# Kernel tuning notes

Measured on AMD Instinct MI355X. Metric: run time of the kernel, lower is better.

## Reference

```python
import jax, jax.numpy as jnp
from jax import lax
import numpy as np

KK = 9          # 3x3 kernel points
BN_EPS = 1e-5


def setup_inputs() -> dict:
    key = jax.random.key(0)
    ks = jax.random.split(key, 8)
    B, C, O, H, W = 4, 256, 256, 64, 64
    x = jax.random.normal(ks[0], (B, C, H, W), jnp.float32)
    # offset/mask conv: 27 = 2*9 offsets + 9 mask logits; small init so offsets are O(1) px
    w_off = jax.random.normal(ks[1], (3 * KK, C, 3, 3), jnp.float32) * 0.01
    b_off = jnp.zeros((3 * KK,), jnp.float32)
    # main deformable conv weight [O, C, 3, 3]
    w = jax.random.normal(ks[2], (O, C, 3, 3), jnp.float32) * (1.0 / np.sqrt(C * KK))
    b = jax.random.normal(ks[3], (O,), jnp.float32) * 0.01
    # BatchNorm (eval mode) params
    gamma = jax.random.uniform(ks[4], (O,), jnp.float32, 0.5, 1.5)
    beta = jax.random.normal(ks[5], (O,), jnp.float32) * 0.1
    running_mean = jax.random.normal(ks[6], (O,), jnp.float32) * 0.1
    running_var = jax.random.uniform(ks[7], (O,), jnp.float32, 0.5, 1.5)
    return dict(x=x, w_off=w_off, b_off=b_off, w=w, b=b, gamma=gamma,
                beta=beta, running_mean=running_mean, running_var=running_var)


def _bilinear_sample(x, py, px):
    """x: [B,C,H,W]; py/px: [B,KK,H,W] float sample coords -> [B,C,KK,H,W]."""
    B, C, H, W = x.shape
    xflat = x.reshape(B, C, H * W)
    y0 = jnp.floor(py)
    x0 = jnp.floor(px)
    ly = py - y0      # frac weights
    lx = px - x0
    y0i = y0.astype(jnp.int32)
    x0i = x0.astype(jnp.int32)

    def corner(yi, xi, wgt):
        valid = (yi >= 0) & (yi < H) & (xi >= 0) & (xi < W)  # zero padding outside
        idx = jnp.clip(yi, 0, H - 1) * W + jnp.clip(xi, 0, W - 1)
        v = jnp.take_along_axis(xflat, idx.reshape(B, 1, -1), axis=2)  # [B,C,KK*H*W]
        return v * (wgt * valid).reshape(B, 1, -1)

    out = (corner(y0i,     x0i,     (1 - ly) * (1 - lx))
           + corner(y0i,     x0i + 1, (1 - ly) * lx)
           + corner(y0i + 1, x0i,     ly * (1 - lx))
           + corner(y0i + 1, x0i + 1, ly * lx))
    return out.reshape(B, C, KK, H, W)


def _deform_conv_bn_relu(x, w_off, b_off, w, b, gamma, beta, running_mean, running_var):
    B, C, H, W = x.shape
    O = w.shape[0]
    # offset/mask branch: plain 3x3 conv, stride 1, pad 1
    om = lax.conv_general_dilated(x, w_off, (1, 1), [(1, 1), (1, 1)])
    om = om + b_off[None, :, None, None]              # [B, 27, H, W]
    off_y = om[:, :KK]                                # DCNv2: o1 -> y offsets
    off_x = om[:, KK:2 * KK]                          # o2 -> x offsets
    mask = jax.nn.sigmoid(om[:, 2 * KK:])             # [B, 9, H, W]

    # base sampling grid for each of the 9 kernel taps (stride 1, pad 1)
    k = jnp.arange(KK)
    ki = (k // 3)[None, :, None, None].astype(jnp.float32)
    kj = (k % 3)[None, :, None, None].astype(jnp.float32)
    hh = jnp.arange(H, dtype=jnp.float32)[None, None, :, None]
    ww = jnp.arange(W, dtype=jnp.float32)[None, None, None, :]
    py = hh - 1.0 + ki + off_y                        # [B,9,H,W]
    px = ww - 1.0 + kj + off_x

    sampled = _bilinear_sample(x, py, px)             # [B,C,9,H,W]
    sampled = sampled * mask[:, None]                 # modulated (DCNv2)

    out = jnp.einsum('bckhw,ock->bohw', sampled, w.reshape(O, C, KK))
    out = out + b[None, :, None, None]

    # BatchNorm (eval / running stats) + ReLU
    inv = gamma / jnp.sqrt(running_var + BN_EPS)
    out = out * inv[None, :, None, None] + (beta - running_mean * inv)[None, :, None, None]
    return jax.nn.relu(out)


def reference(x, w_off, b_off, w, b, gamma, beta, running_mean, running_var):
    return _deform_conv_bn_relu(x, w_off, b_off, w, b, gamma, beta,
                                running_mean, running_var)
```

## Files before the change

kernel.cpp:

```cpp
#include <hip/hip_runtime.h>

#define HH 64
#define WWD 64
#define CIN 256
#define OUTC 256
#define BB 4
#define KK 9
#define NSO2 18
#define QOFF 4
#define NITH 20
#define WROWS 8
#define WPIX 512

typedef __attribute__((ext_vector_type(8))) short short8;
typedef __attribute__((ext_vector_type(4))) short short4v;
typedef __attribute__((ext_vector_type(4))) unsigned short ushort4v;
typedef __attribute__((ext_vector_type(4))) float float4v;

__device__ __forceinline__ short f2bf(float f) {
    unsigned u = __builtin_bit_cast(unsigned, f);
    u += 0x7fffu + ((u >> 16) & 1u);
    return (short)(u >> 16);
}
__device__ __forceinline__ float bf2f(short s) {
    unsigned u = ((unsigned)(unsigned short)s) << 16;
    return __builtin_bit_cast(float, u);
}
__device__ __forceinline__ unsigned cvtpk(float a, float b) {
    unsigned r;
    asm("v_cvt_pk_bf16_f32 %0, %1, %2" : "=v"(r) : "v"(a), "v"(b));
    return r;
}
__device__ __forceinline__ short8 pack8(const float* a) {
    union { short8 s; unsigned u[4]; } r;
    r.u[0] = cvtpk(a[0], a[1]); r.u[1] = cvtpk(a[2], a[3]);
    r.u[2] = cvtpk(a[4], a[5]); r.u[3] = cvtpk(a[6], a[7]);
    return r.s;
}
__device__ __forceinline__ int div9(int s) { return (s * 57) >> 9; }

__global__ __launch_bounds__(256) void k_packs(const float* __restrict__ w,
                                               const float* __restrict__ w_off,
                                               short* __restrict__ wt2,
                                               short* __restrict__ wo2) {
    const int bid = blockIdx.x;
    if (bid < 2304) {
        int gid = bid * 256 + threadIdx.x;
        int kk = gid & 31;
        int o  = (gid >> 5) & 255;
        int s  = gid >> 13;
        int chunk = div9(s), tap = s - 9 * chunk;
        int c = (chunk << 5) + kk;
        wt2[gid] = f2bf(w[(o * CIN + c) * 9 + tap]);
    } else {
        int gid = (bid - 2304) * 256 + threadIdx.x;
        int kk = gid & 31;
        int m  = (gid >> 5) & 31;
        int s  = gid >> 10;
        int chunk = div9(s), tap = s - 9 * chunk;
        int c = (chunk << 5) + kk;
        wo2[gid] = (m < 27) ? f2bf(w_off[(m * CIN + c) * 9 + tap]) : (short)0;
    }
}

__global__ __launch_bounds__(256) void k_off_mfma(const float* __restrict__ x,
                                                  const short* __restrict__ wo2,
                                                  float* __restrict__ om_part) {
    const int wgid = blockIdx.x;
    const int swz  = ((wgid & 7) << 7) + (wgid >> 3);
    const int q = swz & 3;
    const int h = (swz >> 2) & 63;
    const int b = swz >> 8;
    const int tid = threadIdx.x;
    const int lane = tid & 63;
    const int wid  = tid >> 6;

    __shared__ short S[2][4][64][8];

    const int px_t = tid & 63;
    const int g    = tid >> 6;
    const float* xb = x + ((size_t)b << 20);

    float gv[8];
    auto ISSUE = [&](int s2) {
        const int chunk = div9(s2), tap = s2 - 9 * chunk;
        const int gy = h + tap / 3 - 1;
        const int gx = px_t + tap % 3 - 1;
        const bool ok = ((unsigned)gy < 64u) && ((unsigned)gx < 64u);
        const float* xc = xb + (((chunk << 5) + (g << 3)) << 12) + (gy << 6) + gx;
#pragma unroll
        for (int j = 0; j < 8; ++j)
            gv[j] = ok ? xc[(size_t)j << 12] : 0.f;
    };
    auto CONSUME = [&](int buf) {
        short8 p = pack8(gv);
        *(short8*)(&S[buf][g][px_t][0]) = p;
    };

    const int arow = lane & 15;
    const int akk  = (lane >> 4) << 3;
    const int bpx  = lane & 15;
    const int bg   = lane >> 4;

    float4v acc0 = {0.f, 0.f, 0.f, 0.f};
    float4v acc1 = {0.f, 0.f, 0.f, 0.f};

    const int s0 = q * NSO2;
    ISSUE(s0); CONSUME(0); ISSUE(s0 + 1);
    const short* abase = wo2 + (size_t)s0 * 1024 + arow * 32 + akk;
    short8 aC0 = *(const short8*)(abase);
    short8 aC1 = *(const short8*)(abase + 512);
    __syncthreads();

#pragma unroll 1
    for (int ls = 0; ls < NSO2; ++ls) {
        const int lsn = (ls + 1 < NSO2) ? ls + 1 : ls;
        const short* an = wo2 + (size_t)(s0 + lsn) * 1024 + arow * 32 + akk;
        short8 aN0 = *(const short8*)(an);
        short8 aN1 = *(const short8*)(an + 512);

        short8 bf = *(const short8*)(&S[ls & 1][bg][(wid << 4) + bpx][0]);
        acc0 = __builtin_amdgcn_mfma_f32_16x16x32_bf16(aC0, bf, acc0, 0, 0, 0);
        acc1 = __builtin_amdgcn_mfma_f32_16x16x32_bf16(aC1, bf, acc1, 0, 0, 0);

        if (ls < NSO2 - 1) {
            CONSUME((ls + 1) & 1);
            if (ls + 2 < NSO2) ISSUE(s0 + ls + 2);
        }
        aC0 = aN0; aC1 = aN1;
        __syncthreads();
    }

    const int pxo = (wid << 4) + bpx;
    float* ob = om_part + (((size_t)(q * BB + b) * 27) << 12) + (h << 6) + pxo;
#pragma unroll
    for (int r = 0; r < 4; ++r) {
        const int m0 = ((lane >> 4) << 2) + r;
        ob[(size_t)m0 << 12] = acc0[r];
        const int m1 = 16 + m0;
        if (m1 < 27) ob[(size_t)m1 << 12] = acc1[r];
    }
}

__global__ __launch_bounds__(576) void k_params(const float* __restrict__ om_part,
                                                const float* __restrict__ b_off,
                                                unsigned short* __restrict__ sidxG,
                                                unsigned short* __restrict__ swG) {
    const int hb = blockIdx.x;
    const int b = hb >> 6, h = hb & 63;
    const int j = threadIdx.x;
    const int k  = j >> 6;
    const int px = j & 63;
    const int sp = (h << 6) + px;

    float oy = b_off[k], ox = b_off[k + KK], mz = b_off[k + 2 * KK];
#pragma unroll
    for (int qq = 0; qq < QOFF; ++qq) {
        const float* bp = om_part + (size_t)((qq * BB + b) * 27) * 4096 + sp;
        oy += bp[k * 4096];
        ox += bp[(k + KK) * 4096];
        mz += bp[(k + 2 * KK) * 4096];
    }
    const float mask = 1.f / (1.f + expf(-mz));
    const float py  = (float)h  - 1.f + (float)(k / 3) + oy;
    const float pxc = (float)px - 1.f + (float)(k % 3) + ox;
    const float y0f = floorf(py), x0f = floorf(pxc);
    const float ly = py - y0f, lx = pxc - x0f;
    const int y0 = (int)y0f, x0 = (int)x0f;

    float w00, w01, w10, w11;
    {
        bool v = (y0 >= 0) && (y0 < HH) && (x0 >= 0) && (x0 < WWD);
        w00 = v ? (1.f - ly) * (1.f - lx) * mask : 0.f;
    }
    {
        bool v = (y0 >= 0) && (y0 < HH) && (x0 + 1 < WWD) && (x0 + 1 >= 0);
        w01 = v ? (1.f - ly) * lx * mask : 0.f;
    }
    {
        bool v = (y0 + 1 >= 0) && (y0 + 1 < HH) && (x0 >= 0) && (x0 < WWD);
        w10 = v ? ly * (1.f - lx) * mask : 0.f;
    }
    {
        bool v = (y0 + 1 >= 0) && (y0 + 1 < HH) && (x0 + 1 >= 0) && (x0 + 1 < WWD);
        w11 = v ? ly * lx * mask : 0.f;
    }
    const int cy0 = min(max(y0, 0), 63),     cy1 = min(max(y0 + 1, 0), 63);
    const int cx0 = min(max(x0, 0), 63),     cx1 = min(max(x0 + 1, 0), 63);
    const int li0 = cy0 - (h - 3),           li1 = cy1 - (h - 3);
    ushort4v pv;
    if ((unsigned)li0 < (unsigned)WROWS && (unsigned)li1 < (unsigned)WROWS) {
        const int p00 = (li0 << 6) + cx0, p01 = (li0 << 6) + cx1;
        const int p10 = (li1 << 6) + cx0, p11 = (li1 << 6) + cx1;
        pv.x = (unsigned short)((p00 << 6) | ((p00 + (p00 >> 2)) & 3));
        pv.y = (unsigned short)((p01 << 6) | ((p01 + (p01 >> 2)) & 3));
        pv.z = (unsigned short)((p10 << 6) | ((p10 + (p10 >> 2)) & 3));
        pv.w = (unsigned short)((p11 << 6) | ((p11 + (p11 >> 2)) & 3));
    } else {
        pv.x = 0xFFFFu;
        pv.y = (unsigned short)(y0 + 32);
        pv.z = (unsigned short)(x0 + 32);
        pv.w = 0;
    }
    ushort4v wv;
    wv.x = (unsigned short)f2bf(w00);
    wv.y = (unsigned short)f2bf(w01);
    wv.z = (unsigned short)f2bf(w10);
    wv.w = (unsigned short)f2bf(w11);
    ((ushort4v*)sidxG)[hb * 576 + j] = pv;
    ((ushort4v*)swG)[hb * 576 + j]   = wv;
}

__global__ __launch_bounds__(512) void k_main(
    const float* __restrict__ x, const unsigned short* __restrict__ sidxG,
    const unsigned short* __restrict__ swG, const short* __restrict__ wt2,
    float* __restrict__ outr, float* __restrict__ part1) {

    const int wgid = blockIdx.x;
    const int swz  = ((wgid & 7) << 6) + (wgid >> 3);
    const int q = swz & 1;
    const int h = (swz >> 1) & 63;
    const int b = swz >> 7;
    const int tid  = threadIdx.x;
    const int lane = tid & 63;
    const int wid  = tid >> 6;

    __shared__ short S[2][2][4][64][8];
    __shared__ short xw[WPIX * 32];

    const ushort4v* sidx4 = (const ushort4v*)sidxG;
    const ushort4v* sw44  = (const ushort4v*)swG;
    const int pbase = (((b << 6) + h) * 576);

    const float* xb = x + ((size_t)b << 20);

    auto STAGE = [&](int chunk) {
#pragma unroll
        for (int r4 = 0; r4 < 4; ++r4) {
            const int t   = r4 * 512 + tid;
            const int g   = t >> 9;
            const int pix = t & 511;
            const int wr  = pix >> 6, col = pix & 63;
            const int gro = (min(max(h - 3 + wr, 0), 63) << 6) + col;
            const float* xc = xb + ((size_t)((chunk << 5) + (g << 3)) << 12) + gro;
            float a[8];
#pragma unroll
            for (int j = 0; j < 8; ++j) a[j] = xc[(size_t)j << 12];
            short8 p = pack8(a);
            const int pos = (g + pix + (pix >> 2)) & 3;
            *(short8*)&xw[pix * 32 + pos * 8] = p;
        }
    };

    auto SAMPLE = [&](int c2, int sub2, int ntaps2, int buf2) {
        const int tp = tid >> 8;
        if (tp < ntaps2) {
            const int slot = tid & 255;
            const int g  = slot >> 6;
            const int px = slot & 63;
            const int tap = sub2 * 2 + tp;
            const int j = pbase + (tap << 6) + px;
            const ushort4v sv = sidx4[j];
            const ushort4v wv = sw44[j];
            const float w00 = bf2f((short)wv.x), w01 = bf2f((short)wv.y);
            const float w10 = bf2f((short)wv.z), w11 = bf2f((short)wv.w);
            float a[8];
            if (sv.x != 0xFFFFu) {
                const int o0 = ((sv.x & 0xFFC0u) >> 1) + (((sv.x + g) & 3u) << 3);
                const int o1 = ((sv.y & 0xFFC0u) >> 1) + (((sv.y + g) & 3u) << 3);
                const int o2 = ((sv.z & 0xFFC0u) >> 1) + (((sv.z + g) & 3u) << 3);
                const int o3 = ((sv.w & 0xFFC0u) >> 1) + (((sv.w + g) & 3u) << 3);
                const short8 c00 = *(const short8*)&xw[o0];
                const short8 c01 = *(const short8*)&xw[o1];
                const short8 c10 = *(const short8*)&xw[o2];
                const short8 c11 = *(const short8*)&xw[o3];
#pragma unroll
                for (int j2 = 0; j2 < 8; ++j2)
                    a[j2] = w00 * bf2f(c00[j2]) + w01 * bf2f(c01[j2])
                          + w10 * bf2f(c10[j2]) + w11 * bf2f(c11[j2]);
            } else {
                const int y0 = (int)sv.y - 32, x0 = (int)sv.z - 32;
                const int cy0 = min(max(y0, 0), 63), cy1 = min(max(y0 + 1, 0), 63);
                const int cx0 = min(max(x0, 0), 63), cx1 = min(max(x0 + 1, 0), 63);
                const int i00 = (cy0 << 6) + cx0, i01 = (cy0 << 6) + cx1;
                const int i10 = (cy1 << 6) + cx0, i11 = (cy1 << 6) + cx1;
                const float* xc = xb + ((size_t)((c2 << 5) + (g << 3)) << 12);
#pragma unroll
                for (int j2 = 0; j2 < 8; ++j2) {
                    a[j2] = w00 * xc[i00] + w01 * xc[i01]
                          + w10 * xc[i10] + w11 * xc[i11];
                    xc += 4096;
                }
            }
            short8 rr = pack8(a);
            *(short8*)&S[buf2][tp][g][px][0] = rr;
        }
    };

    const short* wbase = wt2 + ((wid * 32 + (lane & 15)) << 5) + ((lane >> 4) << 3);
    const int bpx = lane & 15;
    const int bg  = lane >> 4;

    float4v acc[2][4];
#pragma unroll
    for (int mt = 0; mt < 2; ++mt)
#pragma unroll
        for (int nt = 0; nt < 4; ++nt) acc[mt][nt] = (float4v){0.f, 0.f, 0.f, 0.f};

    const int c0 = q * 4;
    const int sA0 = c0 * 9;

    STAGE(c0);
    __syncthreads();
    SAMPLE(c0, 0, 2, 0);
    short8 aC00 = *(const short8*)(wbase + (size_t)sA0 * 8192);
    short8 aC01 = *(const short8*)(wbase + (size_t)sA0 * 8192 + 512);
    short8 aC10 = *(const short8*)(wbase + (size_t)(sA0 + 1) * 8192);
    short8 aC11 = *(const short8*)(wbase + (size_t)(sA0 + 1) * 8192 + 512);
    __syncthreads();

    int c = c0, sub = 0;
#pragma unroll 1
    for (int it = 0; it < NITH; ++it) {
        const int ntaps = (sub < 4) ? 2 : 1;
        int subn = sub + 1, cn = c;
        if (subn == 5) { subn = 0; cn = c + 1; }
        const int ntapsN = (subn < 4) ? 2 : 1;
        const int sN = cn * 9 + subn * 2;

        short8 aN00 = aC00, aN01 = aC01, aN10 = aC10, aN11 = aC11;
        if (it + 1 < NITH) {
            aN00 = *(const short8*)(wbase + (size_t)sN * 8192);
            aN01 = *(const short8*)(wbase + (size_t)sN * 8192 + 512);
            if (ntapsN == 2) {
                aN10 = *(const short8*)(wbase + (size_t)(sN + 1) * 8192);
                aN11 = *(const short8*)(wbase + (size_t)(sN + 1) * 8192 + 512);
            }
        }

        const int buf = it & 1;
        __builtin_amdgcn_s_setprio(1);
        {
            const short* Sb = &S[buf][0][bg][bpx][0];
            short8 b0 = *(const short8*)(Sb);
            short8 b1 = *(const short8*)(Sb + 128);
            short8 b2 = *(const short8*)(Sb + 256);
            short8 b3 = *(const short8*)(Sb + 384);
            acc[0][0] = __builtin_amdgcn_mfma_f32_16x16x32_bf16(aC00, b0, acc[0][0], 0, 0, 0);
            acc[0][1] = __builtin_amdgcn_mfma_f32_16x16x32_bf16(aC00, b1, acc[0][1], 0, 0, 0);
            acc[0][2] = __builtin_amdgcn_mfma_f32_16x16x32_bf16(aC00, b2, acc[0][2], 0, 0, 0);
            acc[0][3] = __builtin_amdgcn_mfma_f32_16x16x32_bf16(aC00, b3, acc[0][3], 0, 0, 0);
            acc[1][0] = __builtin_amdgcn_mfma_f32_16x16x32_bf16(aC01, b0, acc[1][0], 0, 0, 0);
            acc[1][1] = __builtin_amdgcn_mfma_f32_16x16x32_bf16(aC01, b1, acc[1][1], 0, 0, 0);
            acc[1][2] = __builtin_amdgcn_mfma_f32_16x16x32_bf16(aC01, b2, acc[1][2], 0, 0, 0);
            acc[1][3] = __builtin_amdgcn_mfma_f32_16x16x32_bf16(aC01, b3, acc[1][3], 0, 0, 0);
        }
        if (ntaps == 2) {
            const short* Sb = &S[buf][1][bg][bpx][0];
            short8 b0 = *(const short8*)(Sb);
            short8 b1 = *(const short8*)(Sb + 128);
            short8 b2 = *(const short8*)(Sb + 256);
            short8 b3 = *(const short8*)(Sb + 384);
            acc[0][0] = __builtin_amdgcn_mfma_f32_16x16x32_bf16(aC10, b0, acc[0][0], 0, 0, 0);
            acc[0][1] = __builtin_amdgcn_mfma_f32_16x16x32_bf16(aC10, b1, acc[0][1], 0, 0, 0);
            acc[0][2] = __builtin_amdgcn_mfma_f32_16x16x32_bf16(aC10, b2, acc[0][2], 0, 0, 0);
            acc[0][3] = __builtin_amdgcn_mfma_f32_16x16x32_bf16(aC10, b3, acc[0][3], 0, 0, 0);
            acc[1][0] = __builtin_amdgcn_mfma_f32_16x16x32_bf16(aC11, b0, acc[1][0], 0, 0, 0);
            acc[1][1] = __builtin_amdgcn_mfma_f32_16x16x32_bf16(aC11, b1, acc[1][1], 0, 0, 0);
            acc[1][2] = __builtin_amdgcn_mfma_f32_16x16x32_bf16(aC11, b2, acc[1][2], 0, 0, 0);
            acc[1][3] = __builtin_amdgcn_mfma_f32_16x16x32_bf16(aC11, b3, acc[1][3], 0, 0, 0);
        }
        __builtin_amdgcn_s_setprio(0);

        if (it + 1 < NITH) {
            if (sub == 4) {
                STAGE(cn);
                __syncthreads();
            }
            SAMPLE(cn, subn, ntapsN, (it + 1) & 1);
        }
        aC00 = aN00; aC01 = aN01; aC10 = aN10; aC11 = aN11;
        __syncthreads();
        c = cn; sub = subn;
    }

    const int r4 = lane >> 4;
    float* ob = (q == 0 ? outr : part1) + (((size_t)b * 256) << 12) + (h << 6);
#pragma unroll
    for (int mt = 0; mt < 2; ++mt)
#pragma unroll
        for (int nt = 0; nt < 4; ++nt) {
            const int px = nt * 16 + bpx;
#pragma unroll
            for (int r = 0; r < 4; ++r) {
                const int o = wid * 32 + mt * 16 + r4 * 4 + r;
                ob[((size_t)o << 12) + px] = acc[mt][nt][r];
            }
        }
}

__global__ __launch_bounds__(256) void k_bn(const float* __restrict__ part1,
                                            const float* __restrict__ bias,
                                            const float* __restrict__ gamma,
                                            const float* __restrict__ beta,
                                            const float* __restrict__ rmean,
                                            const float* __restrict__ rvar,
                                            float* __restrict__ out) {
    const int NTOT4 = BB * OUTC * 4096 / 4;
    int i = blockIdx.x * 256 + threadIdx.x;
    const int stride = gridDim.x * 256;
#pragma unroll 1
    for (; i < NTOT4; i += stride) {
        const int e0 = i << 2;
        const int o  = (e0 >> 12) & 255;
        const float inv = gamma[o] * rsqrtf(rvar[o] + 1e-5f);
        const float sh  = beta[o] - rmean[o] * inv + bias[o] * inv;
        float4 a = ((const float4*)out)[i];
        float4 p = ((const float4*)part1)[i];
        float4 v;
        v.x = fmaxf((a.x + p.x) * inv + sh, 0.f);
        v.y = fmaxf((a.y + p.y) * inv + sh, 0.f);
        v.z = fmaxf((a.z + p.z) * inv + sh, 0.f);
        v.w = fmaxf((a.w + p.w) * inv + sh, 0.f);
        ((float4*)out)[i] = v;
    }
}

extern "C" void kernel_launch(void* const* d_in, const int* in_sizes, int n_in,
                              void* d_out, int out_size, void* d_ws, size_t ws_size,
                              hipStream_t stream) {
    const float* x     = (const float*)d_in[0];
    const float* w_off = (const float*)d_in[1];
    const float* b_off = (const float*)d_in[2];
    const float* w     = (const float*)d_in[3];
    const float* bias  = (const float*)d_in[4];
    const float* gamma = (const float*)d_in[5];
    const float* beta  = (const float*)d_in[6];
    const float* rmean = (const float*)d_in[7];
    const float* rvar  = (const float*)d_in[8];
    float* out = (float*)d_out;

    float* om_part = (float*)d_ws;
    short* wt2     = (short*)(om_part + QOFF * BB * 27 * 4096);
    short* wo2     = wt2 + 72 * 256 * 32;
    unsigned short* sidxG = (unsigned short*)(wo2 + 72 * 32 * 32);
    unsigned short* swG   = sidxG + 256 * 576 * 4;
    float* part1   = (float*)(swG + 256 * 576 * 4);

    k_packs<<<2592, 256, 0, stream>>>(w, w_off, wt2, wo2);
    k_off_mfma<<<1024, 256, 0, stream>>>(x, wo2, om_part);
    k_params<<<256, 576, 0, stream>>>(om_part, b_off, sidxG, swG);
    k_main<<<512, 512, 0, stream>>>(x, sidxG, swG, wt2, out, part1);
    k_bn<<<2048, 256, 0, stream>>>(part1, bias, gamma, beta, rmean, rvar, out);
}
```

Baseline: 76.92 us.

## Split main deformable conv channel reduction three ways instead of two

The main kernel now splits the 8 channel chunks across three workgroups per row (3, 3, 2 chunks) instead of two (4, 4), raising the grid from 512 to 768 workgroups. This is meant to fill more compute units on the GPU and shorten each workgroup's serial loop. In exchange it writes a third full-size partial buffer, and the BN epilogue must read and add one more partial. The split is also uneven, so the third group finishes early.

```diff
diff --git a/kernel.cpp b/kernel.cpp
--- a/kernel.cpp
+++ b/kernel.cpp
@@ -8,7 +8,6 @@
 #define KK 9
 #define NSO2 18
 #define QOFF 4
-#define NITH 20
 #define WROWS 8
 #define WPIX 512
 
@@ -214,13 +213,15 @@
 __global__ __launch_bounds__(512) void k_main(
     const float* __restrict__ x, const unsigned short* __restrict__ sidxG,
     const unsigned short* __restrict__ swG, const short* __restrict__ wt2,
-    float* __restrict__ outr, float* __restrict__ part1) {
+    float* __restrict__ outr, float* __restrict__ part1,
+    float* __restrict__ part2) {
 
     const int wgid = blockIdx.x;
-    const int swz  = ((wgid & 7) << 6) + (wgid >> 3);
-    const int q = swz & 1;
-    const int h = (swz >> 1) & 63;
-    const int b = swz >> 7;
+    const int swz  = (wgid & 7) * 96 + (wgid >> 3);
+    const int hb = swz / 3;
+    const int q  = swz - hb * 3;
+    const int h = hb & 63;
+    const int b = hb >> 6;
     const int tid  = threadIdx.x;
     const int lane = tid & 63;
     const int wid  = tid >> 6;
@@ -230,7 +231,7 @@
 
     const ushort4v* sidx4 = (const ushort4v*)sidxG;
     const ushort4v* sw44  = (const ushort4v*)swG;
-    const int pbase = (((b << 6) + h) * 576);
+    const int pbase = hb * 576;
 
     const float* xb = x + ((size_t)b << 20);
 
@@ -307,7 +308,8 @@
 #pragma unroll
         for (int nt = 0; nt < 4; ++nt) acc[mt][nt] = (float4v){0.f, 0.f, 0.f, 0.f};
 
-    const int c0 = q * 4;
+    const int c0  = (q < 2) ? q * 3 : 6;
+    const int nit = (q < 2) ? 15 : 10;
     const int sA0 = c0 * 9;
 
     STAGE(c0);
@@ -321,7 +323,7 @@
 
     int c = c0, sub = 0;
 #pragma unroll 1
-    for (int it = 0; it < NITH; ++it) {
+    for (int it = 0; it < nit; ++it) {
         const int ntaps = (sub < 4) ? 2 : 1;
         int subn = sub + 1, cn = c;
         if (subn == 5) { subn = 0; cn = c + 1; }
@@ -329,7 +331,7 @@
         const int sN = cn * 9 + subn * 2;
 
         short8 aN00 = aC00, aN01 = aC01, aN10 = aC10, aN11 = aC11;
-        if (it + 1 < NITH) {
+        if (it + 1 < nit) {
             aN00 = *(const short8*)(wbase + (size_t)sN * 8192);
             aN01 = *(const short8*)(wbase + (size_t)sN * 8192 + 512);
             if (ntapsN == 2) {
@@ -372,7 +374,7 @@
         }
         __builtin_amdgcn_s_setprio(0);
 
-        if (it + 1 < NITH) {
+        if (it + 1 < nit) {
             if (sub == 4) {
                 STAGE(cn);
                 __syncthreads();
@@ -385,7 +387,8 @@
     }
 
     const int r4 = lane >> 4;
-    float* ob = (q == 0 ? outr : part1) + (((size_t)b * 256) << 12) + (h << 6);
+    float* dst = (q == 0) ? outr : (q == 1 ? part1 : part2);
+    float* ob = dst + (((size_t)b * 256) << 12) + (h << 6);
 #pragma unroll
     for (int mt = 0; mt < 2; ++mt)
 #pragma unroll
@@ -400,6 +403,7 @@
 }
 
 __global__ __launch_bounds__(256) void k_bn(const float* __restrict__ part1,
+                                            const float* __restrict__ part2,
                                             const float* __restrict__ bias,
                                             const float* __restrict__ gamma,
                                             const float* __restrict__ beta,
@@ -417,11 +421,12 @@
         const float sh  = beta[o] - rmean[o] * inv + bias[o] * inv;
         float4 a = ((const float4*)out)[i];
         float4 p = ((const float4*)part1)[i];
+        float4 s = ((const float4*)part2)[i];
         float4 v;
-        v.x = fmaxf((a.x + p.x) * inv + sh, 0.f);
-        v.y = fmaxf((a.y + p.y) * inv + sh, 0.f);
-        v.z = fmaxf((a.z + p.z) * inv + sh, 0.f);
-        v.w = fmaxf((a.w + p.w) * inv + sh, 0.f);
+        v.x = fmaxf((a.x + p.x + s.x) * inv + sh, 0.f);
+        v.y = fmaxf((a.y + p.y + s.y) * inv + sh, 0.f);
+        v.z = fmaxf((a.z + p.z + s.z) * inv + sh, 0.f);
+        v.w = fmaxf((a.w + p.w + s.w) * inv + sh, 0.f);
         ((float4*)out)[i] = v;
     }
 }
@@ -446,10 +451,12 @@
     unsigned short* sidxG = (unsigned short*)(wo2 + 72 * 32 * 32);
     unsigned short* swG   = sidxG + 256 * 576 * 4;
     float* part1   = (float*)(swG + 256 * 576 * 4);
+    float* part2   = part1 + (size_t)BB * 256 * 4096;
 
     k_packs<<<2592, 256, 0, stream>>>(w, w_off, wt2, wo2);
     k_off_mfma<<<1024, 256, 0, stream>>>(x, wo2, om_part);
     k_params<<<256, 576, 0, stream>>>(om_part, b_off, sidxG, swG);
-    k_main<<<512, 512, 0, stream>>>(x, sidxG, swG, wt2, out, part1);
-    k_bn<<<2048, 256, 0, stream>>>(part1, bias, gamma, beta, rmean, rvar, out);
-}
+    k_main<<<768, 512, 0, stream>>>(x, sidxG, swG, wt2, out, part1, part2);
+    k_bn<<<2048, 256, 0, stream>>>(part1, part2, bias, gamma, beta, rmean,
+                                   rvar, out);
+}
```

Measured after the change: 90.75 us. +18.0%, slower.
